# Performance work log

Hardware: AMD Instinct MI355X
Metric: run time of the kernel (lower is better)

## Reference

```python
import jax, jax.numpy as jnp
import numpy as np

NR = 4      # num_real
NC = 6      # num_complex_conjugate_pairs
L = 2       # num_layers (hidden->hidden blocks)
H = 64      # hidden_dim
B, S = 32, 2048
C = NR + 2 * NC


def setup_inputs() -> dict:
    key = jax.random.key(0)
    ks = jax.random.split(key, 9)
    s = 0.1
    return {
        "z": jax.random.normal(ks[0], (B, S, C), jnp.float32),
        "W0_r": jax.random.normal(ks[1], (NR, H), jnp.float32) * s,
        "b0_r": jnp.zeros((NR, H), jnp.float32),
        "Wm_r": jax.random.normal(ks[2], (L, NR, H, H), jnp.float32) * s,
        "bm_r": jnp.zeros((L, NR, H), jnp.float32),
        "Wl_r": jax.random.normal(ks[3], (NR, H, 1), jnp.float32) * s,
        "bl_r": jnp.zeros((NR, 1), jnp.float32),
        "W0_c": jax.random.normal(ks[4], (NC, H), jnp.float32) * s,
        "b0_c": jnp.zeros((NC, H), jnp.float32),
        "Wm_c": jax.random.normal(ks[5], (L, NC, H, H), jnp.float32) * s,
        "bm_c": jnp.zeros((L, NC, H), jnp.float32),
        "Wl_c": jax.random.normal(ks[6], (NC, H, 2), jnp.float32) * s,
        "bl_c": jnp.zeros((NC, 2), jnp.float32),
    }


def _channel_mlps(x, W0, b0, Wm, bm, Wl, bl):
    # x: [F, P] scalar input per channel; runs P independent tiny MLPs.
    h = jax.nn.relu(x[:, :, None] * W0[None] + b0[None])  # [F, P, H]
    for l in range(Wm.shape[0]):  # small fixed layer count
        h = jax.nn.relu(jnp.einsum('fph,phk->fpk', h, Wm[l]) + bm[l][None])
    return jnp.einsum('fph,pho->fpo', h, Wl) + bl[None]  # [F, P, out]


def reference(z, W0_r, b0_r, Wm_r, bm_r, Wl_r, bl_r,
              W0_c, b0_c, Wm_c, bm_c, Wl_c, bl_c):
    b_, s_, c_ = z.shape
    zf = z.reshape(-1, c_)                       # [F, C]
    # real channels
    zr = zf[:, :NR]                              # [F, NR]
    real_lambda = _channel_mlps(zr, W0_r, b0_r, Wm_r, bm_r, Wl_r, bl_r)[..., 0]
    # complex-conjugate pairs
    zc = zf[:, NR:].reshape(-1, NC, 2)           # [F, NC, 2]
    z1, z2 = zc[..., 0], zc[..., 1]
    z_mag = z1 * z1 + z2 * z2                    # [F, NC]
    mo = _channel_mlps(z_mag, W0_c, b0_c, Wm_c, bm_c, Wl_c, bl_c)  # [F, NC, 2]
    mu, omega = mo[..., 0], mo[..., 1]
    mu_exp = jnp.exp(mu)
    mc = mu_exp * jnp.cos(omega)
    ms = mu_exp * jnp.sin(omega)
    # z_pred = z @ K with K block-diagonal: diag(real_lambda) then 2x2 rotations
    out_r = zr * real_lambda                     # [F, NR]
    # row-vector times 2x2 block [[mc, -ms], [ms, mc]]
    o1 = z1 * mc + z2 * ms
    o2 = -z1 * ms + z2 * mc
    out_c = jnp.stack([o1, o2], axis=-1).reshape(-1, 2 * NC)
    return jnp.concatenate([out_r, out_c], axis=-1).reshape(b_, s_, c_)
```

## Files before the change

kernel.cpp:

```cpp
#include <hip/hip_runtime.h>
#include <cstdint>

#define NRC 4
#define NCC 6
#define HD 64
#define CW 16

typedef _Float16 half8 __attribute__((ext_vector_type(8)));
typedef float f32x4 __attribute__((ext_vector_type(4)));

__device__ __forceinline__ uint32_t pkh(float a, float b) {
    auto h = __builtin_amdgcn_cvt_pkrtz(a, b);
    return __builtin_bit_cast(uint32_t, h);
}

__global__ __launch_bounds__(256, 4) void koop_kernel(
    const float* __restrict__ z,
    const float* __restrict__ W0_r, const float* __restrict__ b0_r,
    const float* __restrict__ Wm_r, const float* __restrict__ bm_r,
    const float* __restrict__ Wl_r, const float* __restrict__ bl_r,
    const float* __restrict__ W0_c, const float* __restrict__ b0_c,
    const float* __restrict__ Wm_c, const float* __restrict__ bm_c,
    const float* __restrict__ Wl_c, const float* __restrict__ bl_c,
    float* __restrict__ out)
{
    __shared__ uint32_t smem[10240];

    const int tid  = threadIdx.x;
    const int lane = tid & 63;
    const int wv   = tid >> 6;
    const int bid  = blockIdx.x;
    const int ch   = bid >> 8;
    const int tile = bid & 255;
    const int t0   = tile * 256;

    const bool isReal = (ch < NRC);
    const int  pc     = ch - NRC;
    const int  No     = isReal ? 1 : 2;

    const float* W0 = isReal ? (W0_r + ch * HD) : (W0_c + pc * HD);
    const float* b0 = isReal ? (b0_r + ch * HD) : (b0_c + pc * HD);
    const float* Wl = isReal ? (Wl_r + ch * HD) : (Wl_c + pc * HD * 2);
    const float* bl = isReal ? (bl_r + ch)      : (bl_c + pc * 2);

    {
        const int nH = tid & 63;
        const int bb = (tid >> 6) * 2;
        for (int l = 0; l < 2; ++l) {
            const float* Wm = isReal ? (Wm_r + (l * NRC + ch) * HD * HD)
                                     : (Wm_c + (l * NCC + pc) * HD * HD);
            const int base = l ? 8192 : 0;
            #pragma unroll
            for (int r = 0; r < 2; ++r) {
                const int blk = bb + r;
                const float* src = Wm + blk * 8 * HD + nH;
                float v0 = src[0],       v1 = src[HD],     v2 = src[2*HD], v3 = src[3*HD];
                float v4 = src[4*HD],    v5 = src[5*HD],   v6 = src[6*HD], v7 = src[7*HD];
                const int woff = base + nH * 32 + (((blk + nH) & 7) << 2);
                uint4 q = { pkh(v0, v1), pkh(v2, v3), pkh(v4, v5), pkh(v6, v7) };
                *(uint4*)&smem[woff] = q;
            }
        }
    }
    __syncthreads();

    const int l15 = lane & 15;
    const int g   = lane >> 4;

    half8 A1[4][2];
    #pragma unroll
    for (int m = 0; m < 4; ++m) {
        #pragma unroll
        for (int kt = 0; kt < 2; ++kt) {
            const int row = m * 16 + l15;
            const int blk = kt * 4 + g;
            A1[m][kt] = *(const half8*)&smem[row * 32 + (((blk + row) & 7) << 2)];
        }
    }
    __syncthreads();

    const int t = t0 + wv * 64 + lane;
    float xin = 0.f, z1 = 0.f, z2 = 0.f, sval;
    if (isReal) {
        xin = z[t * CW + ch];
        sval = xin;
    } else {
        float2 zz = *(const float2*)(z + t * CW + NRC + 2 * pc);
        z1 = zz.x; z2 = zz.y;
        sval = z1 * z1 + z2 * z2;
    }

    const int hbase = wv * 2048;
    {
        #pragma unroll
        for (int blk = 0; blk < 8; ++blk) {
            uint32_t q0, q1, q2, q3;
            {
                const int n = blk * 8;
                float a0 = fmaxf(fmaf(sval, W0[n+0], b0[n+0]), 0.f);
                float a1 = fmaxf(fmaf(sval, W0[n+1], b0[n+1]), 0.f);
                float a2 = fmaxf(fmaf(sval, W0[n+2], b0[n+2]), 0.f);
                float a3 = fmaxf(fmaf(sval, W0[n+3], b0[n+3]), 0.f);
                float a4 = fmaxf(fmaf(sval, W0[n+4], b0[n+4]), 0.f);
                float a5 = fmaxf(fmaf(sval, W0[n+5], b0[n+5]), 0.f);
                float a6 = fmaxf(fmaf(sval, W0[n+6], b0[n+6]), 0.f);
                float a7 = fmaxf(fmaf(sval, W0[n+7], b0[n+7]), 0.f);
                q0 = pkh(a0, a1); q1 = pkh(a2, a3); q2 = pkh(a4, a5); q3 = pkh(a6, a7);
            }
            const int woff = hbase + lane * 32 + (((blk + lane) & 7) << 2);
            uint4 q = { q0, q1, q2, q3 };
            *(uint4*)&smem[woff] = q;
        }
    }

    half8 A[4][2];
    #pragma unroll
    for (int m = 0; m < 4; ++m)
        #pragma unroll
        for (int kt = 0; kt < 2; ++kt)
            A[m][kt] = A1[m][kt];

    for (int l = 0; l < 2; ++l) {
        if (l == 1) {
            #pragma unroll
            for (int m = 0; m < 4; ++m) {
                #pragma unroll
                for (int kt = 0; kt < 2; ++kt) {
                    const int row = m * 16 + l15;
                    const int blk = kt * 4 + g;
                    A[m][kt] = *(const half8*)&smem[8192 + row * 32 + (((blk + row) & 7) << 2)];
                }
            }
        }
        const float* bm = isReal ? (bm_r + (l * NRC + ch) * HD)
                                 : (bm_c + (l * NCC + pc) * HD);
        f32x4 bv[4];
        #pragma unroll
        for (int m = 0; m < 4; ++m)
            bv[m] = *(const f32x4*)(bm + m * 16 + g * 4);

        #pragma unroll
        for (int th = 0; th < 2; ++th) {
            f32x4 acc[4][2];
            #pragma unroll
            for (int m = 0; m < 4; ++m)
                #pragma unroll
                for (int u = 0; u < 2; ++u)
                    acc[m][u] = bv[m];

            #pragma unroll
            for (int u = 0; u < 2; ++u) {
                const int tt = th * 2 + u;
                #pragma unroll
                for (int kt = 0; kt < 2; ++kt) {
                    const int row = tt * 16 + l15;
                    const int blk = kt * 4 + g;
                    half8 Bf = *(const half8*)&smem[hbase + row * 32 + (((blk + row) & 7) << 2)];
                    #pragma unroll
                    for (int m = 0; m < 4; ++m)
                        acc[m][u] = __builtin_amdgcn_mfma_f32_16x16x32_f16(A[m][kt], Bf, acc[m][u], 0, 0, 0);
                }
            }

            #pragma unroll
            for (int u = 0; u < 2; ++u) {
                const int tt = th * 2 + u;
                const int row = tt * 16 + l15;
                #pragma unroll
                for (int m = 0; m < 4; ++m) {
                    f32x4 v = acc[m][u];
                    float a0 = fmaxf(v[0], 0.f);
                    float a1 = fmaxf(v[1], 0.f);
                    float a2 = fmaxf(v[2], 0.f);
                    float a3 = fmaxf(v[3], 0.f);
                    const int blk  = 2 * m + (g >> 1);
                    const int woff = hbase + row * 32 + (((blk + row) & 7) << 2) + (g & 1) * 2;
                    uint2 q = { pkh(a0, a1), pkh(a2, a3) };
                    *(uint2*)&smem[woff] = q;
                }
            }
        }
    }

    half8 Af[2];
    #pragma unroll
    for (int kt = 0; kt < 2; ++kt) {
        half8 a;
        #pragma unroll
        for (int e = 0; e < 8; ++e) {
            const int k = kt * 32 + g * 8 + e;
            float w = (l15 < No) ? Wl[k * No + l15] : 0.f;
            a[e] = (_Float16)w;
        }
        Af[kt] = a;
    }
    f32x4 cf0 = (f32x4){0.f, 0.f, 0.f, 0.f};
    if (g == 0) { cf0[0] = bl[0]; if (!isReal) cf0[1] = bl[1]; }
    f32x4 accf[4];
    #pragma unroll
    for (int tt = 0; tt < 4; ++tt) accf[tt] = cf0;
    #pragma unroll
    for (int tt = 0; tt < 4; ++tt) {
        #pragma unroll
        for (int kt = 0; kt < 2; ++kt) {
            const int row = tt * 16 + l15;
            const int blk = kt * 4 + g;
            half8 Bf = *(const half8*)&smem[hbase + row * 32 + (((blk + row) & 7) << 2)];
            accf[tt] = __builtin_amdgcn_mfma_f32_16x16x32_f16(Af[kt], Bf, accf[tt], 0, 0, 0);
        }
    }

    float* smf = (float*)smem;
    const int obase = hbase;
    if (g == 0) {
        #pragma unroll
        for (int tt = 0; tt < 4; ++tt) {
            const int tok = tt * 16 + l15;
            if (isReal) {
                smf[obase + tok * 2] = accf[tt][0];
            } else {
                float2 mo = { accf[tt][0], accf[tt][1] };
                *(float2*)&smf[obase + tok * 2] = mo;
            }
        }
    }
    __asm__ volatile("s_waitcnt lgkmcnt(0)" ::: "memory");
    __builtin_amdgcn_sched_barrier(0);

    if (isReal) {
        float lam = smf[obase + lane * 2];
        out[t * CW + ch] = xin * lam;
    } else {
        float2 mo = *(const float2*)&smf[obase + lane * 2];
        float ex = __expf(mo.x);
        float mc = ex * __cosf(mo.y);
        float ms = ex * __sinf(mo.y);
        float o1 =  z1 * mc + z2 * ms;
        float o2 =  z2 * mc - z1 * ms;
        *(float2*)(out + t * CW + NRC + 2 * pc) = make_float2(o1, o2);
    }
}

extern "C" void kernel_launch(void* const* d_in, const int* in_sizes, int n_in,
                              void* d_out, int out_size, void* d_ws, size_t ws_size,
                              hipStream_t stream) {
    (void)in_sizes; (void)n_in; (void)d_ws; (void)ws_size; (void)out_size;
    const float* z    = (const float*)d_in[0];
    const float* W0_r = (const float*)d_in[1];
    const float* b0_r = (const float*)d_in[2];
    const float* Wm_r = (const float*)d_in[3];
    const float* bm_r = (const float*)d_in[4];
    const float* Wl_r = (const float*)d_in[5];
    const float* bl_r = (const float*)d_in[6];
    const float* W0_c = (const float*)d_in[7];
    const float* b0_c = (const float*)d_in[8];
    const float* Wm_c = (const float*)d_in[9];
    const float* bm_c = (const float*)d_in[10];
    const float* Wl_c = (const float*)d_in[11];
    const float* bl_c = (const float*)d_in[12];
    float* outp = (float*)d_out;

    dim3 grid(2560), block(256);
    koop_kernel<<<grid, block, 0, stream>>>(z, W0_r, b0_r, Wm_r, bm_r, Wl_r, bl_r,
                                            W0_c, b0_c, Wm_c, bm_c, Wl_c, bl_c, outp);
}
```

Before: 26.79 us.

## Process two token tiles per block to amortize weight staging

Each block now handles 512 tokens in two sequential passes instead of 256, halving the grid. The per-block cost of converting and staging the Wm weights into LDS and loading layer-1 fragments is spread over twice as many tokens, and the z loads and final-layer weight fragments are issued up front so their latency overlaps the weight staging. In exchange each block runs longer and the grid has fewer blocks, which reduces parallelism and raises register pressure.

Measured after the change: 46.36 us. +73.1%, slower.

```diff
diff --git a/kernel.cpp b/kernel.cpp
--- a/kernel.cpp
+++ b/kernel.cpp
@@ -30,9 +30,9 @@
     const int lane = tid & 63;
     const int wv   = tid >> 6;
     const int bid  = blockIdx.x;
-    const int ch   = bid >> 8;
-    const int tile = bid & 255;
-    const int t0   = tile * 256;
+    const int ch   = bid >> 7;
+    const int grp  = bid & 127;
+    const int t0   = grp * 512;
 
     const bool isReal = (ch < NRC);
     const int  pc     = ch - NRC;
@@ -42,6 +42,38 @@
     const float* b0 = isReal ? (b0_r + ch * HD) : (b0_c + pc * HD);
     const float* Wl = isReal ? (Wl_r + ch * HD) : (Wl_c + pc * HD * 2);
     const float* bl = isReal ? (bl_r + ch)      : (bl_c + pc * 2);
+
+    const int l15 = lane & 15;
+    const int g   = lane >> 4;
+
+    float xin[2], z1[2], z2[2], sval[2];
+    #pragma unroll
+    for (int it = 0; it < 2; ++it) {
+        const int t = t0 + it * 256 + wv * 64 + lane;
+        if (isReal) {
+            xin[it] = z[t * CW + ch];
+            z1[it] = 0.f; z2[it] = 0.f;
+            sval[it] = xin[it];
+        } else {
+            float2 zz = *(const float2*)(z + t * CW + NRC + 2 * pc);
+            xin[it] = 0.f;
+            z1[it] = zz.x; z2[it] = zz.y;
+            sval[it] = zz.x * zz.x + zz.y * zz.y;
+        }
+    }
+
+    half8 Af[2];
+    #pragma unroll
+    for (int kt = 0; kt < 2; ++kt) {
+        half8 a;
+        #pragma unroll
+        for (int e = 0; e < 8; ++e) {
+            const int k = kt * 32 + g * 8 + e;
+            float w = (l15 < No) ? Wl[k * No + l15] : 0.f;
+            a[e] = (_Float16)w;
+        }
+        Af[kt] = a;
+    }
 
     {
         const int nH = tid & 63;
@@ -54,8 +86,8 @@
             for (int r = 0; r < 2; ++r) {
                 const int blk = bb + r;
                 const float* src = Wm + blk * 8 * HD + nH;
-                float v0 = src[0],       v1 = src[HD],     v2 = src[2*HD], v3 = src[3*HD];
-                float v4 = src[4*HD],    v5 = src[5*HD],   v6 = src[6*HD], v7 = src[7*HD];
+                float v0 = src[0],    v1 = src[HD],   v2 = src[2*HD], v3 = src[3*HD];
+                float v4 = src[4*HD], v5 = src[5*HD], v6 = src[6*HD], v7 = src[7*HD];
                 const int woff = base + nH * 32 + (((blk + nH) & 7) << 2);
                 uint4 q = { pkh(v0, v1), pkh(v2, v3), pkh(v4, v5), pkh(v6, v7) };
                 *(uint4*)&smem[woff] = q;
@@ -63,9 +95,6 @@
         }
     }
     __syncthreads();
-
-    const int l15 = lane & 15;
-    const int g   = lane >> 4;
 
     half8 A1[4][2];
     #pragma unroll
@@ -79,165 +108,144 @@
     }
     __syncthreads();
 
-    const int t = t0 + wv * 64 + lane;
-    float xin = 0.f, z1 = 0.f, z2 = 0.f, sval;
-    if (isReal) {
-        xin = z[t * CW + ch];
-        sval = xin;
-    } else {
-        float2 zz = *(const float2*)(z + t * CW + NRC + 2 * pc);
-        z1 = zz.x; z2 = zz.y;
-        sval = z1 * z1 + z2 * z2;
-    }
-
     const int hbase = wv * 2048;
-    {
-        #pragma unroll
-        for (int blk = 0; blk < 8; ++blk) {
-            uint32_t q0, q1, q2, q3;
-            {
-                const int n = blk * 8;
-                float a0 = fmaxf(fmaf(sval, W0[n+0], b0[n+0]), 0.f);
-                float a1 = fmaxf(fmaf(sval, W0[n+1], b0[n+1]), 0.f);
-                float a2 = fmaxf(fmaf(sval, W0[n+2], b0[n+2]), 0.f);
-                float a3 = fmaxf(fmaf(sval, W0[n+3], b0[n+3]), 0.f);
-                float a4 = fmaxf(fmaf(sval, W0[n+4], b0[n+4]), 0.f);
-                float a5 = fmaxf(fmaf(sval, W0[n+5], b0[n+5]), 0.f);
-                float a6 = fmaxf(fmaf(sval, W0[n+6], b0[n+6]), 0.f);
-                float a7 = fmaxf(fmaf(sval, W0[n+7], b0[n+7]), 0.f);
-                q0 = pkh(a0, a1); q1 = pkh(a2, a3); q2 = pkh(a4, a5); q3 = pkh(a6, a7);
-            }
-            const int woff = hbase + lane * 32 + (((blk + lane) & 7) << 2);
-            uint4 q = { q0, q1, q2, q3 };
-            *(uint4*)&smem[woff] = q;
-        }
-    }
-
-    half8 A[4][2];
-    #pragma unroll
-    for (int m = 0; m < 4; ++m)
-        #pragma unroll
-        for (int kt = 0; kt < 2; ++kt)
-            A[m][kt] = A1[m][kt];
-
-    for (int l = 0; l < 2; ++l) {
-        if (l == 1) {
-            #pragma unroll
-            for (int m = 0; m < 4; ++m) {
-                #pragma unroll
-                for (int kt = 0; kt < 2; ++kt) {
-                    const int row = m * 16 + l15;
-                    const int blk = kt * 4 + g;
-                    A[m][kt] = *(const half8*)&smem[8192 + row * 32 + (((blk + row) & 7) << 2)];
-                }
-            }
-        }
-        const float* bm = isReal ? (bm_r + (l * NRC + ch) * HD)
-                                 : (bm_c + (l * NCC + pc) * HD);
-        f32x4 bv[4];
-        #pragma unroll
-        for (int m = 0; m < 4; ++m)
-            bv[m] = *(const f32x4*)(bm + m * 16 + g * 4);
-
-        #pragma unroll
-        for (int th = 0; th < 2; ++th) {
-            f32x4 acc[4][2];
-            #pragma unroll
-            for (int m = 0; m < 4; ++m)
-                #pragma unroll
-                for (int u = 0; u < 2; ++u)
-                    acc[m][u] = bv[m];
-
-            #pragma unroll
-            for (int u = 0; u < 2; ++u) {
-                const int tt = th * 2 + u;
-                #pragma unroll
-                for (int kt = 0; kt < 2; ++kt) {
-                    const int row = tt * 16 + l15;
-                    const int blk = kt * 4 + g;
-                    half8 Bf = *(const half8*)&smem[hbase + row * 32 + (((blk + row) & 7) << 2)];
-                    #pragma unroll
-                    for (int m = 0; m < 4; ++m)
-                        acc[m][u] = __builtin_amdgcn_mfma_f32_16x16x32_f16(A[m][kt], Bf, acc[m][u], 0, 0, 0);
-                }
-            }
-
-            #pragma unroll
-            for (int u = 0; u < 2; ++u) {
-                const int tt = th * 2 + u;
-                const int row = tt * 16 + l15;
-                #pragma unroll
-                for (int m = 0; m < 4; ++m) {
-                    f32x4 v = acc[m][u];
-                    float a0 = fmaxf(v[0], 0.f);
-                    float a1 = fmaxf(v[1], 0.f);
-                    float a2 = fmaxf(v[2], 0.f);
-                    float a3 = fmaxf(v[3], 0.f);
-                    const int blk  = 2 * m + (g >> 1);
-                    const int woff = hbase + row * 32 + (((blk + row) & 7) << 2) + (g & 1) * 2;
-                    uint2 q = { pkh(a0, a1), pkh(a2, a3) };
-                    *(uint2*)&smem[woff] = q;
-                }
-            }
-        }
-    }
-
-    half8 Af[2];
-    #pragma unroll
-    for (int kt = 0; kt < 2; ++kt) {
-        half8 a;
-        #pragma unroll
-        for (int e = 0; e < 8; ++e) {
-            const int k = kt * 32 + g * 8 + e;
-            float w = (l15 < No) ? Wl[k * No + l15] : 0.f;
-            a[e] = (_Float16)w;
-        }
-        Af[kt] = a;
-    }
-    f32x4 cf0 = (f32x4){0.f, 0.f, 0.f, 0.f};
-    if (g == 0) { cf0[0] = bl[0]; if (!isReal) cf0[1] = bl[1]; }
-    f32x4 accf[4];
-    #pragma unroll
-    for (int tt = 0; tt < 4; ++tt) accf[tt] = cf0;
-    #pragma unroll
-    for (int tt = 0; tt < 4; ++tt) {
-        #pragma unroll
-        for (int kt = 0; kt < 2; ++kt) {
-            const int row = tt * 16 + l15;
-            const int blk = kt * 4 + g;
-            half8 Bf = *(const half8*)&smem[hbase + row * 32 + (((blk + row) & 7) << 2)];
-            accf[tt] = __builtin_amdgcn_mfma_f32_16x16x32_f16(Af[kt], Bf, accf[tt], 0, 0, 0);
-        }
-    }
-
     float* smf = (float*)smem;
     const int obase = hbase;
-    if (g == 0) {
+
+    #pragma unroll
+    for (int it = 0; it < 2; ++it) {
+        const int t = t0 + it * 256 + wv * 64 + lane;
+
+        #pragma unroll
+        for (int blk = 0; blk < 8; ++blk) {
+            const int n = blk * 8;
+            float a0 = fmaxf(fmaf(sval[it], W0[n+0], b0[n+0]), 0.f);
+            float a1 = fmaxf(fmaf(sval[it], W0[n+1], b0[n+1]), 0.f);
+            float a2 = fmaxf(fmaf(sval[it], W0[n+2], b0[n+2]), 0.f);
+            float a3 = fmaxf(fmaf(sval[it], W0[n+3], b0[n+3]), 0.f);
+            float a4 = fmaxf(fmaf(sval[it], W0[n+4], b0[n+4]), 0.f);
+            float a5 = fmaxf(fmaf(sval[it], W0[n+5], b0[n+5]), 0.f);
+            float a6 = fmaxf(fmaf(sval[it], W0[n+6], b0[n+6]), 0.f);
+            float a7 = fmaxf(fmaf(sval[it], W0[n+7], b0[n+7]), 0.f);
+            const int woff = hbase + lane * 32 + (((blk + lane) & 7) << 2);
+            uint4 q = { pkh(a0, a1), pkh(a2, a3), pkh(a4, a5), pkh(a6, a7) };
+            *(uint4*)&smem[woff] = q;
+        }
+
+        half8 A[4][2];
+        #pragma unroll
+        for (int m = 0; m < 4; ++m)
+            #pragma unroll
+            for (int kt = 0; kt < 2; ++kt)
+                A[m][kt] = A1[m][kt];
+
+        for (int l = 0; l < 2; ++l) {
+            if (l == 1) {
+                #pragma unroll
+                for (int m = 0; m < 4; ++m) {
+                    #pragma unroll
+                    for (int kt = 0; kt < 2; ++kt) {
+                        const int row = m * 16 + l15;
+                        const int blk = kt * 4 + g;
+                        A[m][kt] = *(const half8*)&smem[8192 + row * 32 + (((blk + row) & 7) << 2)];
+                    }
+                }
+            }
+            const float* bm = isReal ? (bm_r + (l * NRC + ch) * HD)
+                                     : (bm_c + (l * NCC + pc) * HD);
+            f32x4 bv[4];
+            #pragma unroll
+            for (int m = 0; m < 4; ++m)
+                bv[m] = *(const f32x4*)(bm + m * 16 + g * 4);
+
+            #pragma unroll
+            for (int th = 0; th < 2; ++th) {
+                f32x4 acc[4][2];
+                #pragma unroll
+                for (int m = 0; m < 4; ++m)
+                    #pragma unroll
+                    for (int u = 0; u < 2; ++u)
+                        acc[m][u] = bv[m];
+
+                #pragma unroll
+                for (int u = 0; u < 2; ++u) {
+                    const int tt = th * 2 + u;
+                    #pragma unroll
+                    for (int kt = 0; kt < 2; ++kt) {
+                        const int row = tt * 16 + l15;
+                        const int blk = kt * 4 + g;
+                        half8 Bf = *(const half8*)&smem[hbase + row * 32 + (((blk + row) & 7) << 2)];
+                        #pragma unroll
+                        for (int m = 0; m < 4; ++m)
+                            acc[m][u] = __builtin_amdgcn_mfma_f32_16x16x32_f16(A[m][kt], Bf, acc[m][u], 0, 0, 0);
+                    }
+                }
+
+                #pragma unroll
+                for (int u = 0; u < 2; ++u) {
+                    const int tt = th * 2 + u;
+                    const int row = tt * 16 + l15;
+                    #pragma unroll
+                    for (int m = 0; m < 4; ++m) {
+                        f32x4 v = acc[m][u];
+                        float a0 = fmaxf(v[0], 0.f);
+                        float a1 = fmaxf(v[1], 0.f);
+                        float a2 = fmaxf(v[2], 0.f);
+                        float a3 = fmaxf(v[3], 0.f);
+                        const int blk  = 2 * m + (g >> 1);
+                        const int woff = hbase + row * 32 + (((blk + row) & 7) << 2) + (g & 1) * 2;
+                        uint2 q = { pkh(a0, a1), pkh(a2, a3) };
+                        *(uint2*)&smem[woff] = q;
+                    }
+                }
+            }
+        }
+
+        f32x4 cf0 = (f32x4){0.f, 0.f, 0.f, 0.f};
+        if (g == 0) { cf0[0] = bl[0]; if (!isReal) cf0[1] = bl[1]; }
+        f32x4 accf[4];
+        #pragma unroll
+        for (int tt = 0; tt < 4; ++tt) accf[tt] = cf0;
         #pragma unroll
         for (int tt = 0; tt < 4; ++tt) {
-            const int tok = tt * 16 + l15;
-            if (isReal) {
-                smf[obase + tok * 2] = accf[tt][0];
-            } else {
-                float2 mo = { accf[tt][0], accf[tt][1] };
-                *(float2*)&smf[obase + tok * 2] = mo;
-            }
-        }
-    }
-    __asm__ volatile("s_waitcnt lgkmcnt(0)" ::: "memory");
-    __builtin_amdgcn_sched_barrier(0);
-
-    if (isReal) {
-        float lam = smf[obase + lane * 2];
-        out[t * CW + ch] = xin * lam;
-    } else {
-        float2 mo = *(const float2*)&smf[obase + lane * 2];
-        float ex = __expf(mo.x);
-        float mc = ex * __cosf(mo.y);
-        float ms = ex * __sinf(mo.y);
-        float o1 =  z1 * mc + z2 * ms;
-        float o2 =  z2 * mc - z1 * ms;
-        *(float2*)(out + t * CW + NRC + 2 * pc) = make_float2(o1, o2);
+            #pragma unroll
+            for (int kt = 0; kt < 2; ++kt) {
+                const int row = tt * 16 + l15;
+                const int blk = kt * 4 + g;
+                half8 Bf = *(const half8*)&smem[hbase + row * 32 + (((blk + row) & 7) << 2)];
+                accf[tt] = __builtin_amdgcn_mfma_f32_16x16x32_f16(Af[kt], Bf, accf[tt], 0, 0, 0);
+            }
+        }
+
+        if (g == 0) {
+            #pragma unroll
+            for (int tt = 0; tt < 4; ++tt) {
+                const int tok = tt * 16 + l15;
+                if (isReal) {
+                    smf[obase + tok * 2] = accf[tt][0];
+                } else {
+                    float2 mo = { accf[tt][0], accf[tt][1] };
+                    *(float2*)&smf[obase + tok * 2] = mo;
+                }
+            }
+        }
+        __asm__ volatile("s_waitcnt lgkmcnt(0)" ::: "memory");
+        __builtin_amdgcn_sched_barrier(0);
+
+        if (isReal) {
+            float lam = smf[obase + lane * 2];
+            out[t * CW + ch] = xin[it] * lam;
+        } else {
+            float2 mo = *(const float2*)&smf[obase + lane * 2];
+            float ex = __expf(mo.x);
+            float mc = ex * __cosf(mo.y);
+            float ms = ex * __sinf(mo.y);
+            float o1 =  z1[it] * mc + z2[it] * ms;
+            float o2 =  z2[it] * mc - z1[it] * ms;
+            *(float2*)(out + t * CW + NRC + 2 * pc) = make_float2(o1, o2);
+        }
+        __asm__ volatile("s_waitcnt lgkmcnt(0)" ::: "memory");
+        __builtin_amdgcn_sched_barrier(0);
     }
 }
 
@@ -260,7 +268,7 @@
     const float* bl_c = (const float*)d_in[12];
     float* outp = (float*)d_out;
 
-    dim3 grid(2560), block(256);
+    dim3 grid(1280), block(256);
     koop_kernel<<<grid, block, 0, stream>>>(z, W0_r, b0_r, Wm_r, bm_r, Wl_r, bl_r,
                                             W0_c, b0_c, Wm_c, bm_c, Wl_c, bl_c, outp);
 }
```

## Prepack weights into fp16 fragment layout in prep kernel, use packed fp16 first layer

Applied to the files above, without the earlier changes.

Adds a small prep kernel that converts the hidden weights, output weights and first-layer weights/biases into fp16 and lays them out in MFMA-fragment order in global buffers. The main kernel then loads A fragments directly from those buffers instead of staging and converting them through shared memory per block, which removes two barriers and shrinks LDS so occupancy can rise to 5 blocks. The first layer and the ReLUs now run as packed fp16 math. This adds a second launch per call and lowers first-layer precision to fp16.

Measured after the change: 38.72 us. +44.5%, slower.

```diff
diff --git a/kernel.cpp b/kernel.cpp
--- a/kernel.cpp
+++ b/kernel.cpp
@@ -6,25 +6,92 @@
 #define HD 64
 #define CW 16
 
-typedef _Float16 half8 __attribute__((ext_vector_type(8)));
-typedef float f32x4 __attribute__((ext_vector_type(4)));
+typedef _Float16 half8  __attribute__((ext_vector_type(8)));
+typedef _Float16 half2v __attribute__((ext_vector_type(2)));
+typedef float    f32x4  __attribute__((ext_vector_type(4)));
+
+__device__ uint32_t WMPK[40960];
+__device__ uint32_t WLPK[5120];
+__device__ uint32_t W0PKD[320];
+__device__ uint32_t B0PKD[320];
 
 __device__ __forceinline__ uint32_t pkh(float a, float b) {
     auto h = __builtin_amdgcn_cvt_pkrtz(a, b);
     return __builtin_bit_cast(uint32_t, h);
 }
-
-__global__ __launch_bounds__(256, 4) void koop_kernel(
+__device__ __forceinline__ half2v u2h(uint32_t u) { return __builtin_bit_cast(half2v, u); }
+__device__ __forceinline__ uint32_t h2u(half2v h) { return __builtin_bit_cast(uint32_t, h); }
+
+__device__ __forceinline__ half2v hmax0(half2v h) {
+#if __has_builtin(__builtin_elementwise_max)
+    half2v z = {};
+    return __builtin_elementwise_max(h, z);
+#else
+    half2v r;
+    r[0] = h[0] > (_Float16)0 ? h[0] : (_Float16)0;
+    r[1] = h[1] > (_Float16)0 ? h[1] : (_Float16)0;
+    return r;
+#endif
+}
+__device__ __forceinline__ half2v hfma(half2v a, half2v b, half2v c) {
+#if __has_builtin(__builtin_elementwise_fma)
+    return __builtin_elementwise_fma(a, b, c);
+#else
+    return a * b + c;
+#endif
+}
+
+__global__ void prep_kernel(const float* __restrict__ Wm_r, const float* __restrict__ Wm_c,
+                            const float* __restrict__ Wl_r, const float* __restrict__ Wl_c,
+                            const float* __restrict__ W0_r, const float* __restrict__ W0_c,
+                            const float* __restrict__ b0_r, const float* __restrict__ b0_c)
+{
+    const int gid = blockIdx.x * 256 + threadIdx.x;
+    if (gid < 10240) {
+        const int ch = gid >> 10, rem = gid & 1023;
+        const int l = rem >> 9, frag = rem & 511;
+        const int m = frag & 3, rowsel = frag >> 2;
+        const int l15 = rowsel & 15, kg = rowsel >> 4;
+        const int n = m * 16 + l15;
+        const float* W = (ch < NRC) ? (Wm_r + (l * NRC + ch) * HD * HD)
+                                    : (Wm_c + (l * NCC + (ch - NRC)) * HD * HD);
+        const float* s = W + (kg * 8) * HD + n;
+        uint4 q = { pkh(s[0],      s[HD]),
+                    pkh(s[2*HD],   s[3*HD]),
+                    pkh(s[4*HD],   s[5*HD]),
+                    pkh(s[6*HD],   s[7*HD]) };
+        *(uint4*)&WMPK[gid * 4] = q;
+    } else if (gid < 11520) {
+        const int idx = gid - 10240;
+        const int ch = idx >> 7, frag = idx & 127;
+        const int l15 = frag & 15, kg = frag >> 4;
+        const int No = (ch < NRC) ? 1 : 2;
+        const float* Wl = (ch < NRC) ? (Wl_r + ch * HD) : (Wl_c + (ch - NRC) * HD * 2);
+        float v[8];
+        #pragma unroll
+        for (int e = 0; e < 8; ++e)
+            v[e] = (l15 < No) ? Wl[(kg * 8 + e) * No + l15] : 0.f;
+        uint4 q = { pkh(v[0], v[1]), pkh(v[2], v[3]), pkh(v[4], v[5]), pkh(v[6], v[7]) };
+        *(uint4*)&WLPK[idx * 4] = q;
+    } else if (gid < 12160) {
+        const int idx = gid - 11520;
+        const int which = idx / 320, r = idx % 320;
+        const int ch = r >> 5, j = r & 31;
+        const float* src;
+        if (which == 0) src = (ch < NRC) ? (W0_r + ch * HD) : (W0_c + (ch - NRC) * HD);
+        else            src = (ch < NRC) ? (b0_r + ch * HD) : (b0_c + (ch - NRC) * HD);
+        const uint32_t v = pkh(src[2 * j], src[2 * j + 1]);
+        if (which == 0) W0PKD[r] = v; else B0PKD[r] = v;
+    }
+}
+
+__global__ __launch_bounds__(256, 5) void koop_kernel(
     const float* __restrict__ z,
-    const float* __restrict__ W0_r, const float* __restrict__ b0_r,
-    const float* __restrict__ Wm_r, const float* __restrict__ bm_r,
-    const float* __restrict__ Wl_r, const float* __restrict__ bl_r,
-    const float* __restrict__ W0_c, const float* __restrict__ b0_c,
-    const float* __restrict__ Wm_c, const float* __restrict__ bm_c,
-    const float* __restrict__ Wl_c, const float* __restrict__ bl_c,
+    const float* __restrict__ bm_r, const float* __restrict__ bl_r,
+    const float* __restrict__ bm_c, const float* __restrict__ bl_c,
     float* __restrict__ out)
 {
-    __shared__ uint32_t smem[10240];
+    __shared__ uint32_t smem[8192];
 
     const int tid  = threadIdx.x;
     const int lane = tid & 63;
@@ -36,48 +103,23 @@
 
     const bool isReal = (ch < NRC);
     const int  pc     = ch - NRC;
-    const int  No     = isReal ? 1 : 2;
-
-    const float* W0 = isReal ? (W0_r + ch * HD) : (W0_c + pc * HD);
-    const float* b0 = isReal ? (b0_r + ch * HD) : (b0_c + pc * HD);
-    const float* Wl = isReal ? (Wl_r + ch * HD) : (Wl_c + pc * HD * 2);
-    const float* bl = isReal ? (bl_r + ch)      : (bl_c + pc * 2);
-
-    {
-        const int nH = tid & 63;
-        const int bb = (tid >> 6) * 2;
-        for (int l = 0; l < 2; ++l) {
-            const float* Wm = isReal ? (Wm_r + (l * NRC + ch) * HD * HD)
-                                     : (Wm_c + (l * NCC + pc) * HD * HD);
-            const int base = l ? 8192 : 0;
-            #pragma unroll
-            for (int r = 0; r < 2; ++r) {
-                const int blk = bb + r;
-                const float* src = Wm + blk * 8 * HD + nH;
-                float v0 = src[0],       v1 = src[HD],     v2 = src[2*HD], v3 = src[3*HD];
-                float v4 = src[4*HD],    v5 = src[5*HD],   v6 = src[6*HD], v7 = src[7*HD];
-                const int woff = base + nH * 32 + (((blk + nH) & 7) << 2);
-                uint4 q = { pkh(v0, v1), pkh(v2, v3), pkh(v4, v5), pkh(v6, v7) };
-                *(uint4*)&smem[woff] = q;
-            }
-        }
-    }
-    __syncthreads();
 
     const int l15 = lane & 15;
     const int g   = lane >> 4;
 
+    const uint32_t* wm1 = &WMPK[(ch * 2 + 0) * 2048];
+    const uint32_t* wm2 = &WMPK[(ch * 2 + 1) * 2048];
     half8 A1[4][2];
     #pragma unroll
-    for (int m = 0; m < 4; ++m) {
-        #pragma unroll
-        for (int kt = 0; kt < 2; ++kt) {
-            const int row = m * 16 + l15;
-            const int blk = kt * 4 + g;
-            A1[m][kt] = *(const half8*)&smem[row * 32 + (((blk + row) & 7) << 2)];
-        }
-    }
-    __syncthreads();
+    for (int m = 0; m < 4; ++m)
+        #pragma unroll
+        for (int kt = 0; kt < 2; ++kt)
+            A1[m][kt] = *(const half8*)&wm1[((((kt * 4 + g) * 16 + l15) * 4) + m) * 4];
+
+    half8 Af[2];
+    #pragma unroll
+    for (int kt = 0; kt < 2; ++kt)
+        Af[kt] = *(const half8*)&WLPK[(ch * 128 + (kt * 4 + g) * 16 + l15) * 4];
 
     const int t = t0 + wv * 64 + lane;
     float xin = 0.f, z1 = 0.f, z2 = 0.f, sval;
@@ -92,45 +134,37 @@
 
     const int hbase = wv * 2048;
     {
+        const half2v sv = u2h(pkh(sval, sval));
+        const uint32_t* w0p = &W0PKD[ch * 32];
+        const uint32_t* b0p = &B0PKD[ch * 32];
         #pragma unroll
         for (int blk = 0; blk < 8; ++blk) {
-            uint32_t q0, q1, q2, q3;
-            {
-                const int n = blk * 8;
-                float a0 = fmaxf(fmaf(sval, W0[n+0], b0[n+0]), 0.f);
-                float a1 = fmaxf(fmaf(sval, W0[n+1], b0[n+1]), 0.f);
-                float a2 = fmaxf(fmaf(sval, W0[n+2], b0[n+2]), 0.f);
-                float a3 = fmaxf(fmaf(sval, W0[n+3], b0[n+3]), 0.f);
-                float a4 = fmaxf(fmaf(sval, W0[n+4], b0[n+4]), 0.f);
-                float a5 = fmaxf(fmaf(sval, W0[n+5], b0[n+5]), 0.f);
-                float a6 = fmaxf(fmaf(sval, W0[n+6], b0[n+6]), 0.f);
-                float a7 = fmaxf(fmaf(sval, W0[n+7], b0[n+7]), 0.f);
-                q0 = pkh(a0, a1); q1 = pkh(a2, a3); q2 = pkh(a4, a5); q3 = pkh(a6, a7);
+            uint32_t q[4];
+            #pragma unroll
+            for (int j = 0; j < 4; ++j) {
+                half2v h = hfma(sv, u2h(w0p[blk * 4 + j]), u2h(b0p[blk * 4 + j]));
+                q[j] = h2u(hmax0(h));
             }
             const int woff = hbase + lane * 32 + (((blk + lane) & 7) << 2);
-            uint4 q = { q0, q1, q2, q3 };
-            *(uint4*)&smem[woff] = q;
-        }
-    }
-
-    half8 A[4][2];
-    #pragma unroll
-    for (int m = 0; m < 4; ++m)
-        #pragma unroll
-        for (int kt = 0; kt < 2; ++kt)
-            A[m][kt] = A1[m][kt];
+            uint4 qq = { q[0], q[1], q[2], q[3] };
+            *(uint4*)&smem[woff] = qq;
+        }
+    }
 
     for (int l = 0; l < 2; ++l) {
-        if (l == 1) {
-            #pragma unroll
-            for (int m = 0; m < 4; ++m) {
-                #pragma unroll
-                for (int kt = 0; kt < 2; ++kt) {
-                    const int row = m * 16 + l15;
-                    const int blk = kt * 4 + g;
-                    A[m][kt] = *(const half8*)&smem[8192 + row * 32 + (((blk + row) & 7) << 2)];
-                }
-            }
+        half8 A[4][2];
+        if (l == 0) {
+            #pragma unroll
+            for (int m = 0; m < 4; ++m)
+                #pragma unroll
+                for (int kt = 0; kt < 2; ++kt)
+                    A[m][kt] = A1[m][kt];
+        } else {
+            #pragma unroll
+            for (int m = 0; m < 4; ++m)
+                #pragma unroll
+                for (int kt = 0; kt < 2; ++kt)
+                    A[m][kt] = *(const half8*)&wm2[((((kt * 4 + g) * 16 + l15) * 4) + m) * 4];
         }
         const float* bm = isReal ? (bm_r + (l * NRC + ch) * HD)
                                  : (bm_c + (l * NCC + pc) * HD);
@@ -169,31 +203,18 @@
                 #pragma unroll
                 for (int m = 0; m < 4; ++m) {
                     f32x4 v = acc[m][u];
-                    float a0 = fmaxf(v[0], 0.f);
-                    float a1 = fmaxf(v[1], 0.f);
-                    float a2 = fmaxf(v[2], 0.f);
-                    float a3 = fmaxf(v[3], 0.f);
+                    uint32_t p0 = h2u(hmax0(u2h(pkh(v[0], v[1]))));
+                    uint32_t p1 = h2u(hmax0(u2h(pkh(v[2], v[3]))));
                     const int blk  = 2 * m + (g >> 1);
                     const int woff = hbase + row * 32 + (((blk + row) & 7) << 2) + (g & 1) * 2;
-                    uint2 q = { pkh(a0, a1), pkh(a2, a3) };
+                    uint2 q = { p0, p1 };
                     *(uint2*)&smem[woff] = q;
                 }
             }
         }
     }
 
-    half8 Af[2];
-    #pragma unroll
-    for (int kt = 0; kt < 2; ++kt) {
-        half8 a;
-        #pragma unroll
-        for (int e = 0; e < 8; ++e) {
-            const int k = kt * 32 + g * 8 + e;
-            float w = (l15 < No) ? Wl[k * No + l15] : 0.f;
-            a[e] = (_Float16)w;
-        }
-        Af[kt] = a;
-    }
+    const float* bl = isReal ? (bl_r + ch) : (bl_c + pc * 2);
     f32x4 cf0 = (f32x4){0.f, 0.f, 0.f, 0.f};
     if (g == 0) { cf0[0] = bl[0]; if (!isReal) cf0[1] = bl[1]; }
     f32x4 accf[4];
@@ -260,7 +281,6 @@
     const float* bl_c = (const float*)d_in[12];
     float* outp = (float*)d_out;
 
-    dim3 grid(2560), block(256);
-    koop_kernel<<<grid, block, 0, stream>>>(z, W0_r, b0_r, Wm_r, bm_r, Wl_r, bl_r,
-                                            W0_c, b0_c, Wm_c, bm_c, Wl_c, bl_c, outp);
-}
+    prep_kernel<<<48, 256, 0, stream>>>(Wm_r, Wm_c, Wl_r, Wl_c, W0_r, W0_c, b0_r, b0_c);
+    koop_kernel<<<2560, 256, 0, stream>>>(z, bm_r, bl_r, bm_c, bl_c, outp);
+}
```
